# Performance work log

Hardware: AMD Instinct MI355X
Metric: run time of the kernel (lower is better)

Reference implementation:

```python
import jax, jax.numpy as jnp
import numpy as np
from functools import partial

THRESH = 0.5   # similarity_threshold
EPS = 1e-8     # F.cosine_similarity eps


def setup_inputs() -> dict:
    key = jax.random.key(0)
    # uniform positive vectors -> pairwise cosine ~0.75 > threshold, so merges actually occur
    embeddings = jax.random.uniform(key, (8192, 512), dtype=jnp.float32)
    return {"embeddings": embeddings}


@partial(jax.jit, static_argnums=())
def _greedy_match(embs):
    """One merge round. Returns (partner[i] or -1, consumed-as-j flag per i).
    Faithful to the original greedy: scan i in order; i picks argmax-sim j>i among
    not-yet-merged with sim >= threshold; both get marked merged."""
    n = embs.shape[0]
    norms = jnp.maximum(jnp.linalg.norm(embs, axis=-1), EPS)
    sim = (embs @ embs.T) / (norms[:, None] * norms[None, :])  # [n, n]
    idx = jnp.arange(n)

    def step(merged, xs):
        i, row = xs
        was_consumed = merged[i]
        valid = (~merged) & (idx > i)
        scores = jnp.where(valid, row, -jnp.inf)
        j = jnp.argmax(scores)
        ok = (~was_consumed) & (scores[j] >= THRESH)
        merged = merged.at[i].set(was_consumed | ok)
        merged = merged.at[j].set(merged[j] | ok)
        return merged, (jnp.where(ok, j, -1), was_consumed)

    _, (partners, consumed) = jax.lax.scan(step, jnp.zeros(n, bool), (idx, sim))
    return partners, consumed


def reference(embeddings):
    embs = embeddings
    # outer while-loop mirrors the module: iterate rounds until no merge or n<=1
    while embs.shape[0] > 1:
        partners, consumed = _greedy_match(embs)
        partners_np = np.asarray(partners)
        if not (partners_np >= 0).any():  # merge_occurred == False
            break
        safe = jnp.maximum(partners, 0)
        # fuse_embeddings: clamp(v1 + v2, max=1.0); non-leaders keep their row
        fused = jnp.where((partners >= 0)[:, None],
                          jnp.minimum(embs + embs[safe], 1.0), embs)
        survivors = np.where(~np.asarray(consumed))[0]  # rows not consumed as a j
        embs = fused[survivors]
    return embs
```

## Files before the change

kernel.cpp:

```cpp
#include <hip/hip_runtime.h>
#include <math.h>

#define D 512
#define THRESH 0.5f
#define NMAX 8192
#define TOPK 64
#define INFI 0x7fffffff

typedef short bhalf8 __attribute__((ext_vector_type(8)));
typedef float f32x4 __attribute__((ext_vector_type(4)));

__global__ void k_init(int* dn, int n) { *dn = n; }

__global__ void k_prep(const float* __restrict__ E, float* __restrict__ norms,
                       unsigned short* __restrict__ H, int* __restrict__ partner,
                       const int* __restrict__ dn) {
    int n = *dn;
    int row = blockIdx.x;
    if (row >= n) return;
    int t = threadIdx.x;
    float4 v = ((const float4*)(E + (size_t)row * D))[t];
    float s = v.x * v.x + v.y * v.y + v.z * v.z + v.w * v.w;
    #pragma unroll
    for (int o = 32; o > 0; o >>= 1) s += __shfl_down(s, o, 64);
    __shared__ float ls[2];
    if ((t & 63) == 0) ls[t >> 6] = s;
    float f[4] = {v.x, v.y, v.z, v.w};
    unsigned short r[4];
    #pragma unroll
    for (int u = 0; u < 4; ++u) {
        unsigned int b = __float_as_uint(f[u]);
        r[u] = (unsigned short)((b + 0x7FFFu + ((b >> 16) & 1u)) >> 16);
    }
    uint2 packed;
    packed.x = (unsigned)r[0] | ((unsigned)r[1] << 16);
    packed.y = (unsigned)r[2] | ((unsigned)r[3] << 16);
    *(uint2*)(H + (size_t)row * D + t * 4) = packed;
    if (t == 64) partner[row] = -1;
    __syncthreads();
    if (t == 0) norms[row] = fmaxf(sqrtf(ls[0] + ls[1]), 1e-8f);
}

#define LDSTRIDE 72
__global__ void __launch_bounds__(256) k_mfma_sim(
    const unsigned short* __restrict__ H, const float* __restrict__ norms,
    float* __restrict__ sim, int tile_start, int TR, int simStride,
    const int* __restrict__ dn)
{
    int n = *dn;
    if (tile_start >= n) return;
    int row0 = tile_start + blockIdx.y * 128;
    int col0 = blockIdx.x * 128;
    if (row0 >= n || col0 >= n) return;
    if (col0 + 128 <= row0 + 1) return;

    __shared__ unsigned short As[128 * LDSTRIDE];
    __shared__ unsigned short Bs[128 * LDSTRIDE];
    int tid = threadIdx.x;
    int lane = tid & 63;
    int wave = tid >> 6;
    int wr = wave >> 1;
    int wc = wave & 1;
    int krow = lane & 15;
    int kgrp = (lane >> 4) * 8;

    f32x4 acc[4][4];
    #pragma unroll
    for (int m = 0; m < 4; ++m)
        #pragma unroll
        for (int t = 0; t < 4; ++t)
            acc[m][t] = (f32x4){0.f, 0.f, 0.f, 0.f};

    for (int k0 = 0; k0 < D; k0 += 64) {
        #pragma unroll
        for (int it = 0; it < 4; ++it) {
            int c  = tid + it * 256;
            int rr = c >> 3;
            int cc = c & 7;
            uint4 va = make_uint4(0, 0, 0, 0);
            int gra = row0 + rr;
            if (gra < n) va = *(const uint4*)(H + (size_t)gra * D + k0 + cc * 8);
            *(uint4*)&As[rr * LDSTRIDE + cc * 8] = va;
            uint4 vb = make_uint4(0, 0, 0, 0);
            int grb = col0 + rr;
            if (grb < n) vb = *(const uint4*)(H + (size_t)grb * D + k0 + cc * 8);
            *(uint4*)&Bs[rr * LDSTRIDE + cc * 8] = vb;
        }
        __syncthreads();
        #pragma unroll
        for (int kk = 0; kk < 64; kk += 32) {
            bhalf8 a[4], b[4];
            #pragma unroll
            for (int m = 0; m < 4; ++m)
                a[m] = *(const bhalf8*)&As[(wr * 64 + m * 16 + krow) * LDSTRIDE + kk + kgrp];
            #pragma unroll
            for (int t = 0; t < 4; ++t)
                b[t] = *(const bhalf8*)&Bs[(wc * 64 + t * 16 + krow) * LDSTRIDE + kk + kgrp];
            #pragma unroll
            for (int m = 0; m < 4; ++m)
                #pragma unroll
                for (int t = 0; t < 4; ++t)
                    acc[m][t] = __builtin_amdgcn_mfma_f32_16x16x32_bf16(a[m], b[t], acc[m][t], 0, 0, 0);
        }
        __syncthreads();
    }

    int fcol = lane & 15;
    int frow = (lane >> 4) * 4;
    #pragma unroll
    for (int m = 0; m < 4; ++m) {
        #pragma unroll
        for (int t = 0; t < 4; ++t) {
            #pragma unroll
            for (int v = 0; v < 4; ++v) {
                int gr = row0 + wr * 64 + m * 16 + frow + v;
                int gc = col0 + wc * 64 + t * 16 + fcol;
                if (gr < n && gc < n)
                    sim[(size_t)(gr - tile_start) * simStride + gc] =
                        acc[m][t][v] / (norms[gr] * norms[gc]);
            }
        }
    }
}

__global__ void __launch_bounds__(64) k_topk(
    const float* __restrict__ sim, int tile_start, int TR, int simStride,
    uint2* __restrict__ tkP, int* __restrict__ needFix,
    const int* __restrict__ dn)
{
    int n = *dn;
    int r = blockIdx.x;
    int i = tile_start + r;
    if (r >= TR || i >= n) return;
    int lane = threadIdx.x;
    const float* srow = sim + (size_t)r * simStride;

    float v[8]; int id[8];
    #pragma unroll
    for (int u = 0; u < 8; ++u) { v[u] = -INFINITY; id[u] = INFI; }
    float ovV = -INFINITY; int ovI = INFI;

    for (int j = i + 1 + lane; j < n; j += 64) {
        float x = srow[j];
        if (x > v[7] || (x == v[7] && j < id[7])) {
            if (v[7] > ovV || (v[7] == ovV && id[7] < ovI)) { ovV = v[7]; ovI = id[7]; }
            int p = 7;
            #pragma unroll
            for (int u = 6; u >= 0; --u) {
                bool mv = (x > v[u]) || (x == v[u] && j < id[u]);
                if (mv) { v[u + 1] = v[u]; id[u + 1] = id[u]; p = u; }
            }
            v[p] = x; id[p] = j;
        } else {
            if (x > ovV || (x == ovV && j < ovI)) { ovV = x; ovI = j; }
        }
    }

    int pos = 0;
    float myV = -INFINITY; int myI = INFI;
    for (int k = 0; k < TOPK; ++k) {
        float hv = (pos < 8) ? v[pos] : -INFINITY;
        int   hi = (pos < 8) ? id[pos] : INFI;
        float bv = hv; int bi = hi;
        #pragma unroll
        for (int o = 1; o < 64; o <<= 1) {
            float xv = __shfl_xor(bv, o, 64);
            int   xi = __shfl_xor(bi, o, 64);
            if (xv > bv || (xv == bv && xi < bi)) { bv = xv; bi = xi; }
        }
        if (pos < 8 && hv == bv && hi == bi) pos++;
        if (k == lane) { myV = bv; myI = bi; }
    }
    tkP[(size_t)i * TOPK + lane] = make_uint2(__float_as_uint(myV), (unsigned)myI);

    float v64 = __shfl(myV, 63, 64);
    int   i64 = __shfl(myI, 63, 64);
    float oV = ovV; int oI = ovI;
    #pragma unroll
    for (int o = 1; o < 64; o <<= 1) {
        float xv = __shfl_xor(oV, o, 64);
        int   xi = __shfl_xor(oI, o, 64);
        if (xv > oV || (xv == oV && xi < oI)) { oV = xv; oI = xi; }
    }
    int bad = (oV > v64) || (oV == v64 && oI < i64);
    if (lane == 0) needFix[i] = bad;
}

__global__ void __launch_bounds__(64) k_topkfix(
    const float* __restrict__ sim, int tile_start, int TR, int simStride,
    uint2* __restrict__ tkP, const int* __restrict__ needFix,
    const int* __restrict__ dn)
{
    int n = *dn;
    int r = blockIdx.x;
    int i = tile_start + r;
    if (r >= TR || i >= n) return;
    if (!needFix[i]) return;
    int lane = threadIdx.x;
    __shared__ float lv[64][TOPK];
    __shared__ int   li[64][TOPK];
    for (int u = 0; u < TOPK; ++u) { lv[lane][u] = -INFINITY; li[lane][u] = INFI; }
    const float* srow = sim + (size_t)r * simStride;
    for (int j = i + 1 + lane; j < n; j += 64) {
        float x = srow[j];
        float wv = lv[lane][TOPK - 1]; int wi = li[lane][TOPK - 1];
        if (x > wv || (x == wv && j < wi)) {
            int p = TOPK - 1;
            for (int u = TOPK - 2; u >= 0; --u) {
                float uv = lv[lane][u]; int ui = li[lane][u];
                if (x > uv || (x == uv && j < ui)) { lv[lane][u + 1] = uv; li[lane][u + 1] = ui; p = u; }
                else break;
            }
            lv[lane][p] = x; li[lane][p] = j;
        }
    }
    int pos = 0;
    float myV = -INFINITY; int myI = INFI;
    for (int k = 0; k < TOPK; ++k) {
        float hv = (pos < TOPK) ? lv[lane][pos] : -INFINITY;
        int   hi = (pos < TOPK) ? li[lane][pos] : INFI;
        float bv = hv; int bi = hi;
        #pragma unroll
        for (int o = 1; o < 64; o <<= 1) {
            float xv = __shfl_xor(bv, o, 64);
            int   xi = __shfl_xor(bi, o, 64);
            if (xv > bv || (xv == bv && xi < bi)) { bv = xv; bi = xi; }
        }
        if (pos < TOPK && hv == bv && hi == bi) pos++;
        if (k == lane) { myV = bv; myI = bi; }
    }
    tkP[(size_t)i * TOPK + lane] = make_uint2(__float_as_uint(myV), (unsigned)myI);
}

__device__ __attribute__((noinline)) void sim_fallback(
    int r, int n, int lane, const float* __restrict__ sim, int simStride,
    const unsigned long long* lmask, float& obv, int& obj)
{
    const float* srow = sim + (size_t)r * simStride;
    float bv = -INFINITY; int bj = INFI;
    for (int jb = (r + 1) & ~63; jb < n; jb += 64) {
        int j2 = jb + lane;
        unsigned long long wm = lmask[j2 >> 6];
        bool ok2 = (j2 > r) && (j2 < n) && !((wm >> (j2 & 63)) & 1ull);
        float v2 = ok2 ? srow[j2] : -INFINITY;
        int   i2 = ok2 ? j2 : INFI;
        if (v2 > bv || (v2 == bv && i2 < bj)) { bv = v2; bj = i2; }
    }
    #pragma unroll
    for (int o = 1; o < 64; o <<= 1) {
        float xv = __shfl_xor(bv, o, 64);
        int   xi = __shfl_xor(bj, o, 64);
        if (xv > bv || (xv == bv && xi < bj)) { bv = xv; bj = xi; }
    }
    obv = bv; obj = bj;
}

__device__ __attribute__((noinline)) void dot_fallback(
    int r, int n, int lane, const float* __restrict__ E,
    const float* __restrict__ norms, const unsigned long long* lmask,
    float& obv, int& obj)
{
    float ni = norms[r];
    float4 e0 = *(const float4*)(E + (size_t)r * D + lane * 8);
    float4 e1 = *(const float4*)(E + (size_t)r * D + lane * 8 + 4);
    float bbv = -INFINITY; int bbj = INFI;
    int w0 = (r + 1) >> 6, wN = (n + 63) >> 6;
    for (int ww = w0; ww < wN; ++ww) {
        unsigned long long um = ~lmask[ww];
        if (ww == (r >> 6)) um &= (~0ull) << ((r & 63) + 1);
        int over = (ww << 6) + 64 - n;
        if (over > 0) um &= (over >= 64) ? 0ull : ((~0ull) >> over);
        while (um) {
            int b = __builtin_ctzll(um);
            um &= um - 1;
            int jj = (ww << 6) + b;
            float4 a0 = *(const float4*)(E + (size_t)jj * D + lane * 8);
            float4 a1 = *(const float4*)(E + (size_t)jj * D + lane * 8 + 4);
            float s = e0.x * a0.x + e0.y * a0.y + e0.z * a0.z + e0.w * a0.w
                    + e1.x * a1.x + e1.y * a1.y + e1.z * a1.z + e1.w * a1.w;
            #pragma unroll
            for (int o = 1; o < 64; o <<= 1) s += __shfl_xor(s, o, 64);
            float sv = s / (ni * norms[jj]);
            if (sv > bbv || (sv == bbv && jj < bbj)) { bbv = sv; bbj = jj; }
        }
    }
    obv = bbv; obj = bbj;
}

__global__ void __launch_bounds__(64) k_scan10(
    const uint2* __restrict__ tkP,
    const float* __restrict__ E, const float* __restrict__ norms,
    const float* __restrict__ sim, int simStride, int simOk,
    int* __restrict__ partner, int* __restrict__ srcIdx,
    int* __restrict__ dn)
{
    int n = *dn;
    int lane = threadIdx.x;
    int base_ = lane << 7;

    __shared__ unsigned long long lmask[128];
    __shared__ int wslot[64];
    lmask[lane] = 0ull;
    lmask[64 + lane] = 0ull;

    unsigned long long own0 = 0ull, own1 = 0ull;
    unsigned long long cm0 = 0ull, cm1 = 0ull;

#define WINDOW(U0, U1, LO) {                                                   \
    long long kw_ = (long long)(LO) - base_;                                   \
    if (kw_ > 0) {                                                             \
        if (kw_ >= 128) { U0 = 0ull; U1 = 0ull; }                              \
        else if (kw_ >= 64) { U0 = 0ull; if (kw_ > 64) U1 &= (~0ull) << (int)(kw_ - 64); } \
        else U0 &= (~0ull) << (int)kw_;                                        \
    }                                                                          \
    int kn_ = n - base_;                                                       \
    if (kn_ <= 0) { U0 = 0ull; U1 = 0ull; }                                    \
    else if (kn_ < 64) { U0 &= (~0ull) >> (64 - kn_); U1 = 0ull; }             \
    else if (kn_ < 128) { U1 = (kn_ == 64) ? 0ull : (U1 & ((~0ull) >> (128 - kn_))); } }

#define SETBIT(v) { if (lane == ((v) >> 7)) {                                   \
    if (((v) >> 6) & 1) { own1 |= 1ull << ((v) & 63); lmask[2*lane+1] = own1; } \
    else                { own0 |= 1ull << ((v) & 63); lmask[2*lane]   = own0; } } }
#define SETCMB(v) { if (lane == ((v) >> 7)) {                                   \
    if (((v) >> 6) & 1) cm1 |= 1ull << ((v) & 63);                              \
    else                cm0 |= 1ull << ((v) & 63); } }

    int cursor = 0;
    int guardW = NMAX / 64 + 16;
    while (cursor < n && guardW-- > 0) {
        unsigned long long u0 = ~own0, u1 = ~own1;
        WINDOW(u0, u1, cursor)
        int myCnt = __builtin_popcountll(u0) + __builtin_popcountll(u1);
        int incl = myCnt;
        #pragma unroll
        for (int o = 1; o < 64; o <<= 1) {
            int t = __shfl_up(incl, o, 64);
            if (lane >= o) incl += t;
        }
        int excl = incl - myCnt;
        int total = __builtin_amdgcn_readlane(incl, 63);
        if (total == 0) break;
        if (excl < 64 && myCnt) {
            int rk = excl;
            unsigned long long t0 = u0;
            while (t0 && rk < 64) { int b = __builtin_ctzll(t0); t0 &= t0 - 1; wslot[rk] = base_ + b; ++rk; }
            unsigned long long t1 = u1;
            while (t1 && rk < 64) { int b = __builtin_ctzll(t1); t1 &= t1 - 1; wslot[rk] = base_ + 64 + b; ++rk; }
        }
        int nw = (total < 64) ? total : 64;
        int selR = (lane < nw) ? wslot[lane] : INFI;
        cursor = (total > 64) ? (__builtin_amdgcn_readlane(selR, 63) + 1) : n;

        uint2 c0, c1, c2, c3, c4, c5, c6, c7;
        {
            unsigned sent = 0xFF800000u;
            c0 = c1 = c2 = c3 = c4 = c5 = c6 = c7 = make_uint2(sent, (unsigned)INFI);
            if (selR != INFI) {
                const uint4* p = (const uint4*)(tkP + (size_t)selR * TOPK);
                uint4 g0 = p[0]; uint4 g1 = p[1]; uint4 g2 = p[2]; uint4 g3 = p[3];
                c0 = make_uint2(g0.x, g0.y); c1 = make_uint2(g0.z, g0.w);
                c2 = make_uint2(g1.x, g1.y); c3 = make_uint2(g1.z, g1.w);
                c4 = make_uint2(g2.x, g2.y); c5 = make_uint2(g2.z, g2.w);
                c6 = make_uint2(g3.x, g3.y); c7 = make_uint2(g3.z, g3.w);
            }
        }
        int vld = 0;
        {
            int i0=(int)c0.y, i1=(int)c1.y, i2=(int)c2.y, i3=(int)c3.y;
            int i4=(int)c4.y, i5=(int)c5.y, i6=(int)c6.y, i7=(int)c7.y;
            unsigned long long w0 = lmask[(i0 < n) ? (i0 >> 6) : 0];
            unsigned long long w1 = lmask[(i1 < n) ? (i1 >> 6) : 0];
            unsigned long long w2 = lmask[(i2 < n) ? (i2 >> 6) : 0];
            unsigned long long w3 = lmask[(i3 < n) ? (i3 >> 6) : 0];
            unsigned long long w4 = lmask[(i4 < n) ? (i4 >> 6) : 0];
            unsigned long long w5 = lmask[(i5 < n) ? (i5 >> 6) : 0];
            unsigned long long w6 = lmask[(i6 < n) ? (i6 >> 6) : 0];
            unsigned long long w7 = lmask[(i7 < n) ? (i7 >> 6) : 0];
            vld |= (i0 < n && !((w0 >> (i0 & 63)) & 1ull)) ?   1 : 0;
            vld |= (i1 < n && !((w1 >> (i1 & 63)) & 1ull)) ?   2 : 0;
            vld |= (i2 < n && !((w2 >> (i2 & 63)) & 1ull)) ?   4 : 0;
            vld |= (i3 < n && !((w3 >> (i3 & 63)) & 1ull)) ?   8 : 0;
            vld |= (i4 < n && !((w4 >> (i4 & 63)) & 1ull)) ?  16 : 0;
            vld |= (i5 < n && !((w5 >> (i5 & 63)) & 1ull)) ?  32 : 0;
            vld |= (i6 < n && !((w6 >> (i6 & 63)) & 1ull)) ?  64 : 0;
            vld |= (i7 < n && !((w7 >> (i7 & 63)) & 1ull)) ? 128 : 0;
        }

        unsigned long long act = __ballot(selR != INFI);

        while (act) {
            int L_ = (int)__builtin_ctzll(act);
            act &= act - 1;
            int r_ = __builtin_amdgcn_readlane(selR, L_);
            int vb = __builtin_amdgcn_readlane(vld, L_);
            int j_ = -1; float v_ = -INFINITY;
            if (vb) {
                int t_ = __builtin_ctz((unsigned)vb);
                int jx, vx;
                if (t_ == 0)      { jx = __builtin_amdgcn_readlane((int)c0.y, L_); vx = __builtin_amdgcn_readlane((int)c0.x, L_); }
                else if (t_ == 1) { jx = __builtin_amdgcn_readlane((int)c1.y, L_); vx = __builtin_amdgcn_readlane((int)c1.x, L_); }
                else if (t_ == 2) { jx = __builtin_amdgcn_readlane((int)c2.y, L_); vx = __builtin_amdgcn_readlane((int)c2.x, L_); }
                else if (t_ == 3) { jx = __builtin_amdgcn_readlane((int)c3.y, L_); vx = __builtin_amdgcn_readlane((int)c3.x, L_); }
                else if (t_ == 4) { jx = __builtin_amdgcn_readlane((int)c4.y, L_); vx = __builtin_amdgcn_readlane((int)c4.x, L_); }
                else if (t_ == 5) { jx = __builtin_amdgcn_readlane((int)c5.y, L_); vx = __builtin_amdgcn_readlane((int)c5.x, L_); }
                else if (t_ == 6) { jx = __builtin_amdgcn_readlane((int)c6.y, L_); vx = __builtin_amdgcn_readlane((int)c6.x, L_); }
                else              { jx = __builtin_amdgcn_readlane((int)c7.y, L_); vx = __builtin_amdgcn_readlane((int)c7.x, L_); }
                j_ = jx; v_ = __uint_as_float((unsigned)vx);
            } else {
                uint2 q = tkP[(size_t)r_ * TOPK + lane];
                int ci = (int)q.y;
                unsigned long long wm = lmask[(ci < n) ? (ci >> 6) : 0];
                bool val2 = (ci < n) && !((wm >> (ci & 63)) & 1ull);
                unsigned long long bal2 = __ballot(val2);
                if (bal2) {
                    int L2 = (int)__builtin_ctzll(bal2);
                    j_ = __builtin_amdgcn_readlane(ci, L2);
                    v_ = __uint_as_float((unsigned)__builtin_amdgcn_readlane((int)q.x, L2));
                } else {
                    unsigned long long s0 = ~own0, s1 = ~own1;
                    WINDOW(s0, s1, r_ + 1)
                    if (__ballot((s0 | s1) != 0ull)) {
                        if (simOk) sim_fallback(r_, n, lane, sim, simStride,
                                                (const unsigned long long*)lmask, v_, j_);
                        else       dot_fallback(r_, n, lane, E, norms,
                                                (const unsigned long long*)lmask, v_, j_);
                        if (j_ == INFI) j_ = -1;
                    }
                }
            }
            if (j_ >= 0 && v_ >= THRESH) {
                SETBIT(r_); SETBIT(j_); SETCMB(j_);
                if (lane == 0) partner[r_] = j_;
                act &= ~__ballot(selR == j_);
                int mm = 0;
                mm |= ((int)c0.y == j_) ?   1 : 0;
                mm |= ((int)c1.y == j_) ?   2 : 0;
                mm |= ((int)c2.y == j_) ?   4 : 0;
                mm |= ((int)c3.y == j_) ?   8 : 0;
                mm |= ((int)c4.y == j_) ?  16 : 0;
                mm |= ((int)c5.y == j_) ?  32 : 0;
                mm |= ((int)c6.y == j_) ?  64 : 0;
                mm |= ((int)c7.y == j_) ? 128 : 0;
                vld &= ~mm;
            } else {
                if (lane == 0) partner[r_] = -1;
            }
        }
    }

    {
        int base = lane << 7;
        unsigned long long s0 = ~cm0, s1 = ~cm1;
        int kn = n - base;
        if (kn <= 0) { s0 = 0ull; s1 = 0ull; }
        else if (kn < 64) { s0 &= (~0ull) >> (64 - kn); s1 = 0ull; }
        else if (kn < 128) { s1 = (kn == 64) ? 0ull : (s1 & ((~0ull) >> (128 - kn))); }
        int cnt = __builtin_popcountll(s0) + __builtin_popcountll(s1);
        int inc = cnt;
        #pragma unroll
        for (int o = 1; o < 64; o <<= 1) {
            int t = __shfl_up(inc, o, 64);
            if (lane >= o) inc += t;
        }
        int p = inc - cnt;
        while (s0) { int b = __builtin_ctzll(s0); s0 &= s0 - 1; srcIdx[p++] = base + b; }
        while (s1) { int b = __builtin_ctzll(s1); s1 &= s1 - 1; srcIdx[p++] = base + 64 + b; }
        if (lane == 63) *dn = inc;
    }
#undef WINDOW
#undef SETBIT
#undef SETCMB
}

__global__ void k_fuse(const float* __restrict__ cur, float* __restrict__ nxt,
                       const int* __restrict__ srcIdx, const int* __restrict__ partner,
                       const int* __restrict__ dn) {
    int nn = *dn;
    int k = blockIdx.x;
    if (k >= nn) return;
    int t = threadIdx.x;
    int i = srcIdx[k];
    int p = partner[i];
    float4 v = ((const float4*)(cur + (size_t)i * D))[t];
    if (p >= 0) {
        float4 w = ((const float4*)(cur + (size_t)p * D))[t];
        v.x = fminf(v.x + w.x, 1.0f);
        v.y = fminf(v.y + w.y, 1.0f);
        v.z = fminf(v.z + w.z, 1.0f);
        v.w = fminf(v.w + w.w, 1.0f);
    }
    ((float4*)(nxt + (size_t)k * D))[t] = v;
}

__global__ void k_copyout(const float* __restrict__ src, float* __restrict__ dst, int nelem) {
    int i = blockIdx.x * 256 + threadIdx.x;
    if (i < nelem) dst[i] = src[i];
}

extern "C" void kernel_launch(void* const* d_in, const int* in_sizes, int n_in,
                              void* d_out, int out_size, void* d_ws, size_t ws_size,
                              hipStream_t stream) {
    const float* input = (const float*)d_in[0];
    const int N0 = in_sizes[0] / D;
    char* ws = (char*)d_ws;

    const size_t embA = (size_t)(N0 / 2) * D * sizeof(float);
    const size_t embB = (size_t)(N0 / 4) * D * sizeof(float);
    const size_t embH = (size_t)N0 * D * sizeof(unsigned short);
    float* bufA = (float*)ws;
    float* bufB = (float*)(ws + embA);
    unsigned short* curh = (unsigned short*)(ws + embA + embB);
    char* aux = ws + embA + embB + embH;
    float* norms   = (float*)(aux);
    int*   partner = (int*)(aux + 32 * 1024);
    int*   srcIdx  = (int*)(aux + 96 * 1024);
    int*   dn      = (int*)(aux + 128 * 1024);
    int*   needFix = (int*)(aux + 160 * 1024);
    uint2* tkP     = (uint2*)(aux + 256 * 1024);
    float* simTile = (float*)(aux + 256 * 1024 + (size_t)NMAX * TOPK * 8);
    const size_t fixedBytes = embA + embB + embH + 256 * 1024 + (size_t)NMAX * TOPK * 8;

    int TR = NMAX;
    while (TR > 128 && fixedBytes + (size_t)TR * N0 * sizeof(float) > ws_size) TR >>= 1;
    int simOk = (TR == N0) ? 1 : 0;

    const int ROUNDS = 16;
    k_init<<<1, 1, 0, stream>>>(dn, N0);
    for (int r = 0; r < ROUNDS; ++r) {
        const float* cur = (r == 0) ? input : ((r & 1) ? bufA : bufB);
        float* nxt = (r & 1) ? bufB : bufA;
        k_prep<<<N0, 128, 0, stream>>>(cur, norms, curh, partner, dn);
        int NT = N0 / TR;
        for (int t = 0; t < NT; ++t) {
            dim3 g(N0 / 128, TR / 128);
            k_mfma_sim<<<g, 256, 0, stream>>>(curh, norms, simTile, t * TR, TR, N0, dn);
            k_topk<<<TR, 64, 0, stream>>>(simTile, t * TR, TR, N0, tkP, needFix, dn);
            k_topkfix<<<TR, 64, 0, stream>>>(simTile, t * TR, TR, N0, tkP, needFix, dn);
        }
        k_scan10<<<1, 64, 0, stream>>>(tkP, cur, norms, simTile, N0, simOk, partner, srcIdx, dn);
        k_fuse<<<N0, 128, 0, stream>>>(cur, nxt, srcIdx, partner, dn);
    }
    float* fin = bufB;
    k_copyout<<<(out_size + 255) / 256, 256, 0, stream>>>(fin, (float*)d_out, out_size);
}
```

Baseline: 14.66 ms.

## Resolve greedy scan window in parallel with LDS atomic claims

Replaces the serial per-row readlane loop of the single-wave greedy scan with a parallel claim protocol. Each lane proposes its best unmerged candidate, stamps a shared claim array with atomicMin, and commits the longest conflict-free prefix of lanes in one iteration. Exhausted or conflicting rows fall back to the old serial path. The merged and consumed masks move from per-lane registers into LDS bitmaps updated with atomics. This is meant to cut the latency of the sequential matching step, at the cost of extra LDS atomics, waits and iteration guards, and some risk of diverging from the exact greedy order.

```diff
diff --git a/kernel.cpp b/kernel.cpp
--- a/kernel.cpp
+++ b/kernel.cpp
@@ -287,7 +287,7 @@
     obv = bbv; obj = bbj;
 }
 
-__global__ void __launch_bounds__(64) k_scan10(
+__global__ void __launch_bounds__(64) k_scan11(
     const uint2* __restrict__ tkP,
     const float* __restrict__ E, const float* __restrict__ norms,
     const float* __restrict__ sim, int simStride, int simOk,
@@ -298,13 +298,16 @@
     int lane = threadIdx.x;
     int base_ = lane << 7;
 
-    __shared__ unsigned long long lmask[128];
+    __shared__ unsigned int lmask32[NMAX / 32];
+    __shared__ unsigned int cmask32[NMAX / 32];
+    __shared__ unsigned int claim[NMAX];
     __shared__ int wslot[64];
-    lmask[lane] = 0ull;
-    lmask[64 + lane] = 0ull;
-
-    unsigned long long own0 = 0ull, own1 = 0ull;
-    unsigned long long cm0 = 0ull, cm1 = 0ull;
+    for (int i = lane; i < NMAX / 32; i += 64) { lmask32[i] = 0u; cmask32[i] = 0u; }
+    for (int i = lane; i < NMAX; i += 64) claim[i] = 0xFFFFFFFFu;
+    asm volatile("s_waitcnt lgkmcnt(0)" ::: "memory");
+
+    unsigned wcounter = 0x3FFFFFFu;
+    const unsigned long long* lm64 = (const unsigned long long*)lmask32;
 
 #define WINDOW(U0, U1, LO) {                                                   \
     long long kw_ = (long long)(LO) - base_;                                   \
@@ -318,17 +321,13 @@
     else if (kn_ < 64) { U0 &= (~0ull) >> (64 - kn_); U1 = 0ull; }             \
     else if (kn_ < 128) { U1 = (kn_ == 64) ? 0ull : (U1 & ((~0ull) >> (128 - kn_))); } }
 
-#define SETBIT(v) { if (lane == ((v) >> 7)) {                                   \
-    if (((v) >> 6) & 1) { own1 |= 1ull << ((v) & 63); lmask[2*lane+1] = own1; } \
-    else                { own0 |= 1ull << ((v) & 63); lmask[2*lane]   = own0; } } }
-#define SETCMB(v) { if (lane == ((v) >> 7)) {                                   \
-    if (((v) >> 6) & 1) cm1 |= 1ull << ((v) & 63);                              \
-    else                cm0 |= 1ull << ((v) & 63); } }
-
     int cursor = 0;
-    int guardW = NMAX / 64 + 16;
+    int guardW = NMAX / 32 + 32;
     while (cursor < n && guardW-- > 0) {
-        unsigned long long u0 = ~own0, u1 = ~own1;
+        unsigned a0 = lmask32[4 * lane + 0], a1 = lmask32[4 * lane + 1];
+        unsigned a2 = lmask32[4 * lane + 2], a3 = lmask32[4 * lane + 3];
+        unsigned long long u0 = ~(((unsigned long long)a1 << 32) | a0);
+        unsigned long long u1 = ~(((unsigned long long)a3 << 32) | a2);
         WINDOW(u0, u1, cursor)
         int myCnt = __builtin_popcountll(u0) + __builtin_popcountll(u1);
         int incl = myCnt;
@@ -347,6 +346,7 @@
             unsigned long long t1 = u1;
             while (t1 && rk < 64) { int b = __builtin_ctzll(t1); t1 &= t1 - 1; wslot[rk] = base_ + 64 + b; ++rk; }
         }
+        asm volatile("s_waitcnt lgkmcnt(0)" ::: "memory");
         int nw = (total < 64) ? total : 64;
         int selR = (lane < nw) ? wslot[lane] : INFI;
         cursor = (total > 64) ? (__builtin_amdgcn_readlane(selR, 63) + 1) : n;
@@ -364,93 +364,133 @@
                 c6 = make_uint2(g3.x, g3.y); c7 = make_uint2(g3.z, g3.w);
             }
         }
-        int vld = 0;
-        {
-            int i0=(int)c0.y, i1=(int)c1.y, i2=(int)c2.y, i3=(int)c3.y;
-            int i4=(int)c4.y, i5=(int)c5.y, i6=(int)c6.y, i7=(int)c7.y;
-            unsigned long long w0 = lmask[(i0 < n) ? (i0 >> 6) : 0];
-            unsigned long long w1 = lmask[(i1 < n) ? (i1 >> 6) : 0];
-            unsigned long long w2 = lmask[(i2 < n) ? (i2 >> 6) : 0];
-            unsigned long long w3 = lmask[(i3 < n) ? (i3 >> 6) : 0];
-            unsigned long long w4 = lmask[(i4 < n) ? (i4 >> 6) : 0];
-            unsigned long long w5 = lmask[(i5 < n) ? (i5 >> 6) : 0];
-            unsigned long long w6 = lmask[(i6 < n) ? (i6 >> 6) : 0];
-            unsigned long long w7 = lmask[(i7 < n) ? (i7 >> 6) : 0];
-            vld |= (i0 < n && !((w0 >> (i0 & 63)) & 1ull)) ?   1 : 0;
-            vld |= (i1 < n && !((w1 >> (i1 & 63)) & 1ull)) ?   2 : 0;
-            vld |= (i2 < n && !((w2 >> (i2 & 63)) & 1ull)) ?   4 : 0;
-            vld |= (i3 < n && !((w3 >> (i3 & 63)) & 1ull)) ?   8 : 0;
-            vld |= (i4 < n && !((w4 >> (i4 & 63)) & 1ull)) ?  16 : 0;
-            vld |= (i5 < n && !((w5 >> (i5 & 63)) & 1ull)) ?  32 : 0;
-            vld |= (i6 < n && !((w6 >> (i6 & 63)) & 1ull)) ?  64 : 0;
-            vld |= (i7 < n && !((w7 >> (i7 & 63)) & 1ull)) ? 128 : 0;
-        }
-
-        unsigned long long act = __ballot(selR != INFI);
-
-        while (act) {
-            int L_ = (int)__builtin_ctzll(act);
-            act &= act - 1;
-            int r_ = __builtin_amdgcn_readlane(selR, L_);
-            int vb = __builtin_amdgcn_readlane(vld, L_);
-            int j_ = -1; float v_ = -INFINITY;
-            if (vb) {
-                int t_ = __builtin_ctz((unsigned)vb);
-                int jx, vx;
-                if (t_ == 0)      { jx = __builtin_amdgcn_readlane((int)c0.y, L_); vx = __builtin_amdgcn_readlane((int)c0.x, L_); }
-                else if (t_ == 1) { jx = __builtin_amdgcn_readlane((int)c1.y, L_); vx = __builtin_amdgcn_readlane((int)c1.x, L_); }
-                else if (t_ == 2) { jx = __builtin_amdgcn_readlane((int)c2.y, L_); vx = __builtin_amdgcn_readlane((int)c2.x, L_); }
-                else if (t_ == 3) { jx = __builtin_amdgcn_readlane((int)c3.y, L_); vx = __builtin_amdgcn_readlane((int)c3.x, L_); }
-                else if (t_ == 4) { jx = __builtin_amdgcn_readlane((int)c4.y, L_); vx = __builtin_amdgcn_readlane((int)c4.x, L_); }
-                else if (t_ == 5) { jx = __builtin_amdgcn_readlane((int)c5.y, L_); vx = __builtin_amdgcn_readlane((int)c5.x, L_); }
-                else if (t_ == 6) { jx = __builtin_amdgcn_readlane((int)c6.y, L_); vx = __builtin_amdgcn_readlane((int)c6.x, L_); }
-                else              { jx = __builtin_amdgcn_readlane((int)c7.y, L_); vx = __builtin_amdgcn_readlane((int)c7.x, L_); }
-                j_ = jx; v_ = __uint_as_float((unsigned)vx);
-            } else {
-                uint2 q = tkP[(size_t)r_ * TOPK + lane];
-                int ci = (int)q.y;
-                unsigned long long wm = lmask[(ci < n) ? (ci >> 6) : 0];
-                bool val2 = (ci < n) && !((wm >> (ci & 63)) & 1ull);
-                unsigned long long bal2 = __ballot(val2);
-                if (bal2) {
-                    int L2 = (int)__builtin_ctzll(bal2);
-                    j_ = __builtin_amdgcn_readlane(ci, L2);
-                    v_ = __uint_as_float((unsigned)__builtin_amdgcn_readlane((int)q.x, L2));
-                } else {
-                    unsigned long long s0 = ~own0, s1 = ~own1;
-                    WINDOW(s0, s1, r_ + 1)
-                    if (__ballot((s0 | s1) != 0ull)) {
-                        if (simOk) sim_fallback(r_, n, lane, sim, simStride,
-                                                (const unsigned long long*)lmask, v_, j_);
-                        else       dot_fallback(r_, n, lane, E, norms,
-                                                (const unsigned long long*)lmask, v_, j_);
-                        if (j_ == INFI) j_ = -1;
+
+        wcounter--;
+        unsigned stampCur = wcounter << 6;
+        bool resolved = (selR == INFI);
+
+        int guardI = 700;
+        while (guardI-- > 0) {
+            unsigned long long unres = __ballot(!resolved);
+            if (!unres) break;
+
+            bool rowMerged = false;
+            int vld = 0;
+            if (!resolved) {
+                unsigned wrw = lmask32[selR >> 5];
+                rowMerged = (wrw >> (selR & 31)) & 1u;
+            }
+            if (!resolved && !rowMerged) {
+#define CHK(ck, bit) { int ci_ = (int)ck.y; if (ci_ < n) {                      \
+                unsigned wm_ = lmask32[ci_ >> 5];                               \
+                if (!((wm_ >> (ci_ & 31)) & 1u)) vld |= bit; } }
+                CHK(c0, 1) CHK(c1, 2) CHK(c2, 4) CHK(c3, 8)
+                CHK(c4, 16) CHK(c5, 32) CHK(c6, 64) CHK(c7, 128)
+#undef CHK
+            }
+            if (!resolved && rowMerged) resolved = true;
+
+            int pj = INFI; float pvf = -INFINITY;
+            bool exhausted = false;
+            if (!resolved) {
+                if (vld) {
+                    int t_ = __builtin_ctz((unsigned)vld);
+                    int jx, vx;
+                    if (t_ == 0)      { jx = (int)c0.y; vx = (int)c0.x; }
+                    else if (t_ == 1) { jx = (int)c1.y; vx = (int)c1.x; }
+                    else if (t_ == 2) { jx = (int)c2.y; vx = (int)c2.x; }
+                    else if (t_ == 3) { jx = (int)c3.y; vx = (int)c3.x; }
+                    else if (t_ == 4) { jx = (int)c4.y; vx = (int)c4.x; }
+                    else if (t_ == 5) { jx = (int)c5.y; vx = (int)c5.x; }
+                    else if (t_ == 6) { jx = (int)c6.y; vx = (int)c6.x; }
+                    else              { jx = (int)c7.y; vx = (int)c7.x; }
+                    pj = jx; pvf = __uint_as_float((unsigned)vx);
+                    if (pvf < THRESH) resolved = true;
+                } else exhausted = true;
+            }
+
+            bool claiming = (!resolved && vld != 0);
+            unsigned stampLane = stampCur | (unsigned)lane;
+            if (claiming) atomicMin(&claim[pj], stampLane);
+            asm volatile("s_waitcnt lgkmcnt(0)" ::: "memory");
+
+            bool won = false, rowStamped = false;
+            int rcLane = 64;
+            if (claiming) won = (claim[pj] == stampLane);
+            if (!resolved) {
+                unsigned rc = claim[selR];
+                rowStamped = ((rc >> 6) == wcounter);
+                rcLane = (int)(rc & 63u);
+            }
+
+            bool hard = !resolved && (exhausted || (claiming && !won));
+            unsigned long long hb = __ballot(hard);
+            int T = hb ? (int)__builtin_ctzll(hb) : 64;
+            bool commit = claiming && won && !rowStamped && (lane < T);
+            if (commit) {
+                atomicOr(&lmask32[selR >> 5], 1u << (selR & 31));
+                atomicOr(&lmask32[pj >> 5], 1u << (pj & 31));
+                atomicOr(&cmask32[pj >> 5], 1u << (pj & 31));
+                partner[selR] = pj;
+                resolved = true;
+            }
+            unsigned long long cb = __ballot(commit);
+            if (!resolved && rowStamped && rcLane < 64 && ((cb >> rcLane) & 1ull)) {
+                if (claiming && won) claim[pj] = 0xFFFFFFFFu;
+                resolved = true;
+            }
+            asm volatile("s_waitcnt lgkmcnt(0)" ::: "memory");
+
+            unsigned long long su = __ballot(!resolved);
+            if (su) {
+                int Fu = (int)__builtin_ctzll(su);
+                int fex = __builtin_amdgcn_readlane((int)(exhausted ? 1 : 0), Fu);
+                if (fex) {
+                    int r_ = __builtin_amdgcn_readlane(selR, Fu);
+                    uint2 q = tkP[(size_t)r_ * TOPK + lane];
+                    int ci = (int)q.y;
+                    unsigned wm = lmask32[(ci < n) ? (ci >> 5) : 0];
+                    bool val2 = (ci < n) && !((wm >> (ci & 31)) & 1u);
+                    unsigned long long bal2 = __ballot(val2);
+                    int j_ = -1; float v_ = -INFINITY;
+                    if (bal2) {
+                        int L2 = (int)__builtin_ctzll(bal2);
+                        j_ = __builtin_amdgcn_readlane(ci, L2);
+                        v_ = __uint_as_float((unsigned)__builtin_amdgcn_readlane((int)q.x, L2));
+                    } else {
+                        unsigned b0 = lmask32[4 * lane + 0], b1 = lmask32[4 * lane + 1];
+                        unsigned b2 = lmask32[4 * lane + 2], b3 = lmask32[4 * lane + 3];
+                        unsigned long long s0 = ~(((unsigned long long)b1 << 32) | b0);
+                        unsigned long long s1 = ~(((unsigned long long)b3 << 32) | b2);
+                        WINDOW(s0, s1, r_ + 1)
+                        if (__ballot((s0 | s1) != 0ull)) {
+                            if (simOk) sim_fallback(r_, n, lane, sim, simStride, lm64, v_, j_);
+                            else       dot_fallback(r_, n, lane, E, norms, lm64, v_, j_);
+                            if (j_ == INFI) j_ = -1;
+                        }
                     }
+                    if (j_ >= 0 && v_ >= THRESH) {
+                        if (lane == 0) {
+                            atomicOr(&lmask32[r_ >> 5], 1u << (r_ & 31));
+                            atomicOr(&lmask32[j_ >> 5], 1u << (j_ & 31));
+                            atomicOr(&cmask32[j_ >> 5], 1u << (j_ & 31));
+                            partner[r_] = j_;
+                        }
+                    }
+                    if (lane == Fu) resolved = true;
+                    asm volatile("s_waitcnt lgkmcnt(0)" ::: "memory");
                 }
             }
-            if (j_ >= 0 && v_ >= THRESH) {
-                SETBIT(r_); SETBIT(j_); SETCMB(j_);
-                if (lane == 0) partner[r_] = j_;
-                act &= ~__ballot(selR == j_);
-                int mm = 0;
-                mm |= ((int)c0.y == j_) ?   1 : 0;
-                mm |= ((int)c1.y == j_) ?   2 : 0;
-                mm |= ((int)c2.y == j_) ?   4 : 0;
-                mm |= ((int)c3.y == j_) ?   8 : 0;
-                mm |= ((int)c4.y == j_) ?  16 : 0;
-                mm |= ((int)c5.y == j_) ?  32 : 0;
-                mm |= ((int)c6.y == j_) ?  64 : 0;
-                mm |= ((int)c7.y == j_) ? 128 : 0;
-                vld &= ~mm;
-            } else {
-                if (lane == 0) partner[r_] = -1;
-            }
         }
     }
 
     {
+        asm volatile("s_waitcnt lgkmcnt(0)" ::: "memory");
+        unsigned d0 = cmask32[4 * lane + 0], d1 = cmask32[4 * lane + 1];
+        unsigned d2 = cmask32[4 * lane + 2], d3 = cmask32[4 * lane + 3];
+        unsigned long long s0 = ~(((unsigned long long)d1 << 32) | d0);
+        unsigned long long s1 = ~(((unsigned long long)d3 << 32) | d2);
         int base = lane << 7;
-        unsigned long long s0 = ~cm0, s1 = ~cm1;
         int kn = n - base;
         if (kn <= 0) { s0 = 0ull; s1 = 0ull; }
         else if (kn < 64) { s0 &= (~0ull) >> (64 - kn); s1 = 0ull; }
@@ -468,8 +508,6 @@
         if (lane == 63) *dn = inc;
     }
 #undef WINDOW
-#undef SETBIT
-#undef SETCMB
 }
 
 __global__ void k_fuse(const float* __restrict__ cur, float* __restrict__ nxt,
@@ -537,7 +575,7 @@
             k_topk<<<TR, 64, 0, stream>>>(simTile, t * TR, TR, N0, tkP, needFix, dn);
             k_topkfix<<<TR, 64, 0, stream>>>(simTile, t * TR, TR, N0, tkP, needFix, dn);
         }
-        k_scan10<<<1, 64, 0, stream>>>(tkP, cur, norms, simTile, N0, simOk, partner, srcIdx, dn);
+        k_scan11<<<1, 64, 0, stream>>>(tkP, cur, norms, simTile, N0, simOk, partner, srcIdx, dn);
         k_fuse<<<N0, 128, 0, stream>>>(cur, nxt, srcIdx, partner, dn);
     }
     float* fin = bufB;
```

New measurement: 13.82 ms. -5.8%, faster.
